# Performance work log

Measured on AMD Instinct MI355X. Metric: run time of the kernel, lower is better.

## Reference

```python
import jax, jax.numpy as jnp
import numpy as np

NUM_HEADS = 16
EPS = 1e-6  # LinearAttention.epsilon

def setup_inputs() -> dict:
    key = jax.random.key(0)
    ks = jax.random.split(key, 10)
    B, L, D = 4, 4096, 2048
    s = 1.0 / np.sqrt(D)
    x = jax.random.normal(ks[0], (B, L, D), dtype=jnp.float32)
    attention_mask = jnp.ones((B, L), dtype=jnp.float32)
    Wq = jax.random.normal(ks[1], (D, D), dtype=jnp.float32) * s
    bq = jnp.zeros((D,), dtype=jnp.float32)
    Wk = jax.random.normal(ks[2], (D, D), dtype=jnp.float32) * s
    bk = jnp.zeros((D,), dtype=jnp.float32)
    Wv = jax.random.normal(ks[3], (D, D), dtype=jnp.float32) * s
    bv = jnp.zeros((D,), dtype=jnp.float32)
    Wo = jax.random.normal(ks[4], (D, D), dtype=jnp.float32) * s
    bo = jnp.zeros((D,), dtype=jnp.float32)
    return {"x": x, "attention_mask": attention_mask, "Wq": Wq, "bq": bq,
            "Wk": Wk, "bk": bk, "Wv": Wv, "bv": bv, "Wo": Wo, "bo": bo}

def reference(x, attention_mask, Wq, bq, Wk, bk, Wv, bv, Wo, bo):
    B, L, Dm = x.shape
    H = NUM_HEADS
    Dh = Dm // H
    # q/k/v projections -> [B, H, L, Dh]
    def proj(W, b):
        return (x @ W + b).reshape(B, L, H, Dh).transpose(0, 2, 1, 3)
    q = proj(Wq, bq)
    k = proj(Wk, bk)
    v = proj(Wv, bv)
    # feature map: elu(x) + 1
    q = jax.nn.elu(q) + 1.0
    k = jax.nn.elu(k) + 1.0
    # mask keys/values: mask [B, 1, L, 1]
    m = attention_mask[:, None, :, None]
    k = k * m
    v = v * m
    # causal linear attention via cumulative sums over sequence dim
    k_cum = jnp.cumsum(k, axis=2)          # [B,H,L,Dh]
    kv_cum = jnp.cumsum(k * v, axis=2)     # [B,H,L,Dh] (diagonal kv state, as in source)
    z = jnp.sum(q * k_cum, axis=-1) + EPS  # [B,H,L]
    z = z * attention_mask[:, None, :]
    out = (q * kv_cum) / z[..., None]      # [B,H,L,Dh]
    out = out.transpose(0, 2, 1, 3).reshape(B, L, Dm)
    return out @ Wo + bo
```

## Files before the change

### kernel.cpp

```cpp
#include <hip/hip_runtime.h>
#include <cstdint>
#include <cstddef>

#define EPS_F 1e-6f

__device__ inline unsigned short f2bf(float f) {
    union { float f; unsigned u; } v; v.f = f;
    unsigned r = v.u + 0x7fffu + ((v.u >> 16) & 1u);
    return (unsigned short)(r >> 16);
}
__device__ inline float bf2f(unsigned u16) {
    union { unsigned u; float f; } v; v.u = u16 << 16; return v.f;
}

typedef __attribute__((ext_vector_type(8))) __bf16 bf16x8;
typedef __attribute__((ext_vector_type(8))) short short8;
typedef __attribute__((ext_vector_type(8))) unsigned short ushort8;
typedef __attribute__((ext_vector_type(4))) float floatx4;
typedef __attribute__((ext_vector_type(4))) unsigned uintx4;

__device__ inline void async_load16(const void* g, void* l) {
    __builtin_amdgcn_global_load_lds((const __attribute__((address_space(1))) void*)g,
                                     (__attribute__((address_space(3))) void*)l,
                                     16, 0, 0);
}

#define LDS_OFF(p) ((unsigned)(unsigned long long)(const __attribute__((address_space(3))) void*)(p))

__global__ void cast_x_kernel(const float* __restrict__ in, unsigned short* __restrict__ out, int n8) {
    int i = blockIdx.x * blockDim.x + threadIdx.x;
    if (i < n8) {
        float4 a = ((const float4*)in)[2 * i];
        float4 b = ((const float4*)in)[2 * i + 1];
        short8 o;
        o[0] = (short)f2bf(a.x); o[1] = (short)f2bf(a.y);
        o[2] = (short)f2bf(a.z); o[3] = (short)f2bf(a.w);
        o[4] = (short)f2bf(b.x); o[5] = (short)f2bf(b.y);
        o[6] = (short)f2bf(b.z); o[7] = (short)f2bf(b.w);
        ((short8*)out)[i] = o;
    }
}

__global__ void transpose_cast_kernel(const float* __restrict__ W0, const float* __restrict__ W1,
                                      const float* __restrict__ W2, const float* __restrict__ W3,
                                      unsigned short* __restrict__ WtBase, int n) {
    const float* W = (blockIdx.z == 0) ? W0 : (blockIdx.z == 1) ? W1 : (blockIdx.z == 2) ? W2 : W3;
    unsigned short* Wt = WtBase + (size_t)blockIdx.z * n * n;
    __shared__ float tile[32][33];
    int bx = blockIdx.x * 32;
    int by = blockIdx.y * 32;
    int tx = threadIdx.x;
    int ty = threadIdx.y;
    #pragma unroll
    for (int i = 0; i < 32; i += 8)
        tile[ty + i][tx] = W[(size_t)(by + ty + i) * n + bx + tx];
    __syncthreads();
    #pragma unroll
    for (int i = 0; i < 32; i += 8)
        Wt[(size_t)(bx + ty + i) * n + by + tx] = f2bf(tile[tx][ty + i]);
}

#define BMT 256
#define BNT 256
#define BKT 32
#define SLOT_ELEMS (BMT * BKT)
#define DMODEL 2048

template<int FINAL>
__global__ __launch_bounds__(512, 2)
void gemm_kernel(const unsigned short* __restrict__ A,
                 const unsigned short* __restrict__ Bt,
                 const float* __restrict__ b0, const float* __restrict__ b1,
                 const float* __restrict__ b2,
                 const float* __restrict__ mask,
                 unsigned short* __restrict__ qo, unsigned short* __restrict__ ko,
                 unsigned short* __restrict__ vo,
                 float* __restrict__ Cf,
                 int M, int K) {
    __shared__ __align__(16) unsigned short As[4 * SLOT_ELEMS];
    __shared__ __align__(16) unsigned short Bs[4 * SLOT_ELEMS];

    const int tid  = threadIdx.x;
    const int lane = tid & 63;
    const int wave = tid >> 6;
    const int wr   = wave >> 2;
    const int wc   = wave & 3;
    const int quad  = lane >> 4;
    const int row16 = lane & 15;

    const int nwg = (int)(gridDim.x * gridDim.y);
    const int bid = (int)(blockIdx.y * gridDim.x + blockIdx.x);
    const int cpx = nwg >> 3;
    const int swz = (bid & 7) * cpx + (bid >> 3);
    const int bm  = swz % (int)gridDim.x;
    const int bn  = swz / (int)gridDim.x;

    const int m0    = bm * BMT;
    const int nglob = bn * BNT;
    int mat = 0, n0 = nglob;
    const float* bias = b0;
    unsigned short* Cb = nullptr;
    if (!FINAL) {
        mat  = nglob >> 11;
        n0   = nglob & (DMODEL - 1);
        bias = (mat == 0) ? b0 : (mat == 1) ? b1 : b2;
        Cb   = (mat == 0) ? qo : (mat == 1) ? ko : vo;
    }

    floatx4 acc[8][4] = {};

    const unsigned short* gA[2];
    const unsigned short* gB[2];
    #pragma unroll
    for (int b = 0; b < 2; b++) {
        int s = b * 512 + tid;
        int r = s >> 2, c = s & 3;
        int cg = c ^ ((r >> 1) & 3);
        gA[b] = A  + (size_t)(m0 + r) * K + cg * 8;
        gB[b] = Bt + (size_t)(nglob + r) * K + cg * 8;
    }

    const unsigned asB = LDS_OFF(As);
    const unsigned bsB = LDS_OFF(Bs);
    const unsigned cP    = (unsigned)(quad ^ ((row16 >> 1) & 3));
    const unsigned aLane = asB + (unsigned)(wr * 8192 + row16 * 64) + cP * 16u;
    const unsigned bLane = bsB + (unsigned)(wc * 4096 + row16 * 64) + cP * 16u;

    auto stage = [&](int tt, int sl) {
        const int koff = tt * BKT;
        #pragma unroll
        for (int b = 0; b < 2; b++) {
            int s = b * 512 + tid;
            async_load16(gA[b] + koff, As + sl * SLOT_ELEMS + s * 8);
            async_load16(gB[b] + koff, Bs + sl * SLOT_ELEMS + s * 8);
        }
    };

    const int NT = K / BKT;
    stage(0, 0); stage(1, 1); stage(2, 2);

    for (int t = 0; t < NT; ++t) {
        const int slot = t & 3;
        if (t < NT - 2)       asm volatile("s_waitcnt vmcnt(8)" ::: "memory");
        else if (t == NT - 2) asm volatile("s_waitcnt vmcnt(4)" ::: "memory");
        else                  asm volatile("s_waitcnt vmcnt(0)" ::: "memory");
        __builtin_amdgcn_s_barrier();
        asm volatile("" ::: "memory");
        if (t + 3 < NT) stage(t + 3, (t + 3) & 3);

        const unsigned aOff = aLane + (unsigned)slot * (SLOT_ELEMS * 2);
        const unsigned bOff = bLane + (unsigned)slot * (SLOT_ELEMS * 2);
        uintx4 araw[8], braw[4];
        #pragma unroll
        for (int i = 0; i < 8; i++)
            asm volatile("ds_read_b128 %0, %1" : "=v"(araw[i]) : "v"(aOff + (unsigned)(i * 1024)));
        #pragma unroll
        for (int j = 0; j < 4; j++)
            asm volatile("ds_read_b128 %0, %1" : "=v"(braw[j]) : "v"(bOff + (unsigned)(j * 1024)));
        asm volatile("s_waitcnt lgkmcnt(0)");
        __builtin_amdgcn_sched_barrier(0);
        __builtin_amdgcn_s_setprio(1);
        #pragma unroll
        for (int i = 0; i < 8; i++) {
            bf16x8 af = __builtin_bit_cast(bf16x8, araw[i]);
            #pragma unroll
            for (int j = 0; j < 4; j++)
                acc[i][j] = __builtin_amdgcn_mfma_f32_16x16x32_bf16(
                    af, __builtin_bit_cast(bf16x8, braw[j]), acc[i][j], 0, 0, 0);
        }
        __builtin_amdgcn_s_setprio(0);
    }

    float bcache[4];
    #pragma unroll
    for (int j = 0; j < 4; j++) bcache[j] = bias[n0 + wc * 64 + j * 16 + row16];
    #pragma unroll
    for (int i = 0; i < 8; i++) {
        #pragma unroll
        for (int r = 0; r < 4; r++) {
            int row = m0 + wr * 128 + i * 16 + quad * 4 + r;
            float mr = 1.0f;
            if (!FINAL && mat >= 1) mr = mask[row];
            #pragma unroll
            for (int j = 0; j < 4; j++) {
                int col = n0 + wc * 64 + j * 16 + row16;
                float v = acc[i][j][r] + bcache[j];
                if (FINAL) {
                    Cf[(size_t)row * DMODEL + col] = v;
                } else {
                    if (mat <= 1) v = (v > 0.f) ? (v + 1.f) : __expf(v);
                    v *= mr;
                    Cb[(size_t)row * DMODEL + col] = f2bf(v);
                }
            }
        }
    }
}

#define SL    4096
#define SD    2048
#define SH    16
#define CHUNK 64
#define NCH   64

__global__ void scan_partial_kernel(const unsigned short* __restrict__ k,
                                    const unsigned short* __restrict__ v,
                                    float* __restrict__ sumK, float* __restrict__ sumKV) {
    int blk = blockIdx.x;
    int c = blk & (NCH - 1), bh = blk >> 6;
    int b = bh >> 4, h = bh & (SH - 1);
    int lane = threadIdx.x;
    int tg = lane >> 4, dg = lane & 15;
    size_t base = ((size_t)(b * SL + c * CHUNK + tg)) * SD + h * 128 + dg * 8;
    float sk[8] = {0.f, 0.f, 0.f, 0.f, 0.f, 0.f, 0.f, 0.f};
    float skv[8] = {0.f, 0.f, 0.f, 0.f, 0.f, 0.f, 0.f, 0.f};
    for (int it = 0; it < CHUNK / 4; it++) {
        ushort8 kw = *(const ushort8*)(k + base);
        ushort8 vw = *(const ushort8*)(v + base);
        #pragma unroll
        for (int j = 0; j < 8; j++) {
            float kf = bf2f(kw[j]);
            float vf = bf2f(vw[j]);
            sk[j] += kf; skv[j] += kf * vf;
        }
        base += (size_t)4 * SD;
    }
    #pragma unroll
    for (int j = 0; j < 8; j++) {
        sk[j]  += __shfl_xor(sk[j], 16);  sk[j]  += __shfl_xor(sk[j], 32);
        skv[j] += __shfl_xor(skv[j], 16); skv[j] += __shfl_xor(skv[j], 32);
    }
    if (tg == 0) {
        size_t o = ((size_t)bh * NCH + c) * 128 + dg * 8;
        *(float4*)(sumK  + o)     = make_float4(sk[0], sk[1], sk[2], sk[3]);
        *(float4*)(sumK  + o + 4) = make_float4(sk[4], sk[5], sk[6], sk[7]);
        *(float4*)(sumKV + o)     = make_float4(skv[0], skv[1], skv[2], skv[3]);
        *(float4*)(sumKV + o + 4) = make_float4(skv[4], skv[5], skv[6], skv[7]);
    }
}

__global__ void scan_offsets_kernel(const float* __restrict__ sumK, const float* __restrict__ sumKV,
                                    float* __restrict__ offK, float* __restrict__ offKV) {
    int bh = blockIdx.x;
    int d  = threadIdx.x;
    float aK = 0.f, aKV = 0.f;
    for (int c = 0; c < NCH; c++) {
        size_t o = ((size_t)bh * NCH + c) * 128 + d;
        float sk = sumK[o], skv = sumKV[o];
        offK[o] = aK; offKV[o] = aKV;
        aK += sk; aKV += skv;
    }
}

__global__ void scan_final_kernel(const unsigned short* __restrict__ q,
                                  const unsigned short* __restrict__ k,
                                  const unsigned short* __restrict__ v,
                                  const float* __restrict__ offK, const float* __restrict__ offKV,
                                  const float* __restrict__ mask,
                                  unsigned short* __restrict__ out) {
    int blk = blockIdx.x;
    int c = blk & (NCH - 1), bh = blk >> 6;
    int b = bh >> 4, h = bh & (SH - 1);
    int lane = threadIdx.x;
    size_t ob = ((size_t)bh * NCH + c) * 128 + 2 * lane;
    float2 kcv = *(const float2*)(offK  + ob);
    float2 kvv = *(const float2*)(offKV + ob);
    float kc0 = kcv.x, kc1 = kcv.y, kv0 = kvv.x, kv1 = kvv.y;
    size_t base = ((size_t)(b * SL + c * CHUNK)) * SD + h * 128 + 2 * lane;
    const float* mrow = mask + (size_t)b * SL + c * CHUNK;
    for (int s = 0; s < CHUNK / 4; s++) {
        unsigned kw[4], vw[4], qw[4];
        #pragma unroll
        for (int u = 0; u < 4; u++) {
            size_t a = base + (size_t)u * SD;
            kw[u] = *(const unsigned*)(k + a);
            vw[u] = *(const unsigned*)(v + a);
            qw[u] = *(const unsigned*)(q + a);
        }
        float p[4], n0[4], n1[4];
        #pragma unroll
        for (int u = 0; u < 4; u++) {
            float kk0 = bf2f(kw[u] & 0xffff), kk1 = bf2f(kw[u] >> 16);
            float vv0 = bf2f(vw[u] & 0xffff), vv1 = bf2f(vw[u] >> 16);
            float qq0 = bf2f(qw[u] & 0xffff), qq1 = bf2f(qw[u] >> 16);
            kc0 += kk0; kc1 += kk1;
            kv0 += kk0 * vv0; kv1 += kk1 * vv1;
            p[u]  = qq0 * kc0 + qq1 * kc1;
            n0[u] = qq0 * kv0; n1[u] = qq1 * kv1;
        }
        #pragma unroll
        for (int off = 32; off > 0; off >>= 1) {
            #pragma unroll
            for (int u = 0; u < 4; u++) p[u] += __shfl_xor(p[u], off);
        }
        #pragma unroll
        for (int u = 0; u < 4; u++) {
            float z = (p[u] + EPS_F) * mrow[s * 4 + u];
            float inv = 1.0f / z;
            unsigned o0 = f2bf(n0[u] * inv);
            unsigned o1 = f2bf(n1[u] * inv);
            *(unsigned*)(out + base + (size_t)u * SD) = o0 | (o1 << 16);
        }
        base += (size_t)4 * SD;
    }
}

extern "C" void kernel_launch(void* const* d_in, const int* in_sizes, int n_in,
                              void* d_out, int out_size, void* d_ws, size_t ws_size,
                              hipStream_t stream) {
    const float* x  = (const float*)d_in[0];
    const float* am = (const float*)d_in[1];
    const float* Wq = (const float*)d_in[2];
    const float* bq = (const float*)d_in[3];
    const float* Wk = (const float*)d_in[4];
    const float* bk = (const float*)d_in[5];
    const float* Wv = (const float*)d_in[6];
    const float* bv = (const float*)d_in[7];
    const float* Wo = (const float*)d_in[8];
    const float* bo = (const float*)d_in[9];
    float* out = (float*)d_out;

    const int Bb = 4, L = 4096, D = 2048;
    const int M = Bb * L;
    const size_t MD = (size_t)M * D;

    char* w = (char*)d_ws;
    unsigned short* xb    = (unsigned short*)w; w += MD * 2;
    unsigned short* qb    = (unsigned short*)w; w += MD * 2;
    unsigned short* kb    = (unsigned short*)w; w += MD * 2;
    unsigned short* vb    = (unsigned short*)w; w += MD * 2;
    unsigned short* WT    = (unsigned short*)w; w += (size_t)4 * D * D * 2;
    float* sumK  = (float*)w; w += (size_t)64 * NCH * 128 * 4;
    float* sumKV = (float*)w; w += (size_t)64 * NCH * 128 * 4;
    float* offK  = (float*)w; w += (size_t)64 * NCH * 128 * 4;
    float* offKV = (float*)w; w += (size_t)64 * NCH * 128 * 4;
    unsigned short* attnb = xb;

    int n8 = (int)(MD / 8);
    cast_x_kernel<<<(n8 + 255) / 256, 256, 0, stream>>>(x, xb, n8);
    dim3 tb(32, 8);
    dim3 tg(D / 32, D / 32, 4);
    transpose_cast_kernel<<<tg, tb, 0, stream>>>(Wq, Wk, Wv, Wo, WT, D);

    dim3 gq(M / BMT, 3 * D / BNT);
    gemm_kernel<0><<<gq, 512, 0, stream>>>(xb, WT, bq, bk, bv, am, qb, kb, vb, nullptr, M, D);

    scan_partial_kernel<<<64 * NCH, 64, 0, stream>>>(kb, vb, sumK, sumKV);
    scan_offsets_kernel<<<64, 128, 0, stream>>>(sumK, sumKV, offK, offKV);
    scan_final_kernel<<<64 * NCH, 64, 0, stream>>>(qb, kb, vb, offK, offKV, am, attnb);

    dim3 go(M / BMT, D / BNT);
    gemm_kernel<1><<<go, 512, 0, stream>>>(attnb, WT + (size_t)3 * D * D, bo, nullptr, nullptr,
                                           nullptr, nullptr, nullptr, nullptr, out, M, D);
}
```

Measured before the change: 911.6 us.

## Software-pipeline LDS fragment reads across k-steps to overlap with MFMA

Restructures the GEMM main loop so the LDS fragment reads for the next k-tile are issued while the current tile's MFMAs run. A-fragments are split into two halves and B-fragments are double-buffered in registers, with the loop unrolled by two to alternate buffers. The aim is to hide ds_read latency, which the old loop exposed by waiting on lgkmcnt(0) before any MFMA. It raises register pressure and changes the vmcnt/barrier timing, and it assumes NT is even.

```diff
diff --git a/kernel.cpp b/kernel.cpp
--- a/kernel.cpp
+++ b/kernel.cpp
@@ -64,7 +64,57 @@
 #define BNT 256
 #define BKT 32
 #define SLOT_ELEMS (BMT * BKT)
+#define SLOT_BYTES 16384
 #define DMODEL 2048
+
+#define DSR(dst, base, OFF) \
+    asm volatile("ds_read_b128 %0, %1 offset:" OFF : "=v"(dst) : "v"(base) : "memory")
+#define READ_A0(f, base) { DSR(f[0], base, "0");    DSR(f[1], base, "1024"); \
+                           DSR(f[2], base, "2048"); DSR(f[3], base, "3072"); }
+#define READ_A1(f, base) { DSR(f[0], base, "4096"); DSR(f[1], base, "5120"); \
+                           DSR(f[2], base, "6144"); DSR(f[3], base, "7168"); }
+#define READ_B(f, base)  { DSR(f[0], base, "0");    DSR(f[1], base, "1024"); \
+                           DSR(f[2], base, "2048"); DSR(f[3], base, "3072"); }
+
+#define MFMA_HALF(i0, af, bf)                                                   \
+    _Pragma("unroll")                                                           \
+    for (int i_ = 0; i_ < 4; i_++) {                                            \
+        bf16x8 a_ = __builtin_bit_cast(bf16x8, af[i_]);                         \
+        _Pragma("unroll")                                                       \
+        for (int j_ = 0; j_ < 4; j_++)                                          \
+            acc[i0 + i_][j_] = __builtin_amdgcn_mfma_f32_16x16x32_bf16(         \
+                a_, __builtin_bit_cast(bf16x8, bf[j_]), acc[i0 + i_][j_], 0, 0, 0); \
+    }
+
+#define GEMM_ITER(T, BCUR, BNXT)                                                \
+  {                                                                             \
+    const int T_ = (T);                                                         \
+    if (T_ <= NT - 3)      asm volatile("s_waitcnt vmcnt(4)" ::: "memory");     \
+    else if (T_ == NT - 2) asm volatile("s_waitcnt vmcnt(0)" ::: "memory");     \
+    __builtin_amdgcn_s_barrier();                                               \
+    __builtin_amdgcn_sched_barrier(0);                                          \
+    if (T_ + 3 < NT) stage(T_ + 3, (T_ + 3) & 3);                               \
+    asm volatile("s_waitcnt lgkmcnt(4)" ::: "memory");                          \
+    __builtin_amdgcn_sched_barrier(0);                                          \
+    __builtin_amdgcn_s_setprio(1);                                              \
+    MFMA_HALF(0, af0, BCUR);                                                    \
+    __builtin_amdgcn_s_setprio(0);                                              \
+    const int tn_ = T_ + 1;                                                     \
+    const unsigned aN_ = aLane + (unsigned)((tn_ & 3) * SLOT_BYTES);            \
+    const unsigned bN_ = bLane + (unsigned)((tn_ & 3) * SLOT_BYTES);            \
+    if (tn_ < NT) {                                                             \
+      READ_A0(af0, aN_);                                                        \
+      READ_B(BNXT, bN_);                                                        \
+      asm volatile("s_waitcnt lgkmcnt(8)" ::: "memory");                        \
+    } else {                                                                    \
+      asm volatile("s_waitcnt lgkmcnt(0)" ::: "memory");                        \
+    }                                                                           \
+    __builtin_amdgcn_sched_barrier(0);                                          \
+    __builtin_amdgcn_s_setprio(1);                                              \
+    MFMA_HALF(4, af1, BCUR);                                                    \
+    __builtin_amdgcn_s_setprio(0);                                              \
+    if (tn_ < NT) { READ_A1(af1, aN_); }                                        \
+  }
 
 template<int FINAL>
 __global__ __launch_bounds__(512, 2)
@@ -138,37 +188,18 @@
 
     const int NT = K / BKT;
     stage(0, 0); stage(1, 1); stage(2, 2);
-
-    for (int t = 0; t < NT; ++t) {
-        const int slot = t & 3;
-        if (t < NT - 2)       asm volatile("s_waitcnt vmcnt(8)" ::: "memory");
-        else if (t == NT - 2) asm volatile("s_waitcnt vmcnt(4)" ::: "memory");
-        else                  asm volatile("s_waitcnt vmcnt(0)" ::: "memory");
-        __builtin_amdgcn_s_barrier();
-        asm volatile("" ::: "memory");
-        if (t + 3 < NT) stage(t + 3, (t + 3) & 3);
-
-        const unsigned aOff = aLane + (unsigned)slot * (SLOT_ELEMS * 2);
-        const unsigned bOff = bLane + (unsigned)slot * (SLOT_ELEMS * 2);
-        uintx4 araw[8], braw[4];
-        #pragma unroll
-        for (int i = 0; i < 8; i++)
-            asm volatile("ds_read_b128 %0, %1" : "=v"(araw[i]) : "v"(aOff + (unsigned)(i * 1024)));
-        #pragma unroll
-        for (int j = 0; j < 4; j++)
-            asm volatile("ds_read_b128 %0, %1" : "=v"(braw[j]) : "v"(bOff + (unsigned)(j * 1024)));
-        asm volatile("s_waitcnt lgkmcnt(0)");
-        __builtin_amdgcn_sched_barrier(0);
-        __builtin_amdgcn_s_setprio(1);
-        #pragma unroll
-        for (int i = 0; i < 8; i++) {
-            bf16x8 af = __builtin_bit_cast(bf16x8, araw[i]);
-            #pragma unroll
-            for (int j = 0; j < 4; j++)
-                acc[i][j] = __builtin_amdgcn_mfma_f32_16x16x32_bf16(
-                    af, __builtin_bit_cast(bf16x8, braw[j]), acc[i][j], 0, 0, 0);
-        }
-        __builtin_amdgcn_s_setprio(0);
+    asm volatile("s_waitcnt vmcnt(8)" ::: "memory");
+    __builtin_amdgcn_s_barrier();
+    __builtin_amdgcn_sched_barrier(0);
+
+    uintx4 af0[4], af1[4], bfE[4], bfO[4];
+    READ_A0(af0, aLane);
+    READ_B(bfE, bLane);
+    READ_A1(af1, aLane);
+
+    for (int t = 0; t < NT; t += 2) {
+        GEMM_ITER(t,     bfE, bfO);
+        GEMM_ITER(t + 1, bfO, bfE);
     }
 
     float bcache[4];
```

Result: faster. 889.2 us (-2.5%).
